# Kernel optimization log

Hardware: AMD Instinct MI355X
Metric: run time of the kernel (lower is better)

The kernel has to match this reference:

```python
import jax, jax.numpy as jnp
import numpy as np

N = 100000   # nodes
E = 800000   # directed edges
IN = 256     # in_channels (== hidden, required by repo's vn MLP dims)
HID = 256    # hidden_channels
OUT = 40     # out_channels (arxiv classes)
EPS = 1e-5


def setup_inputs() -> dict:
    key = jax.random.key(0)
    ks = jax.random.split(key, 8)
    def nrm(k, shape, scale=0.05):
        return jax.random.normal(k, shape, dtype=jnp.float32) * scale
    return {
        "x": nrm(ks[0], (N, IN), 1.0),
        "edge_index": jax.random.randint(ks[1], (2, E), 0, N, dtype=jnp.int32),
        # GCNConv weights (PyG: x @ W, then normalized aggregation, then + bias)
        "W0": nrm(ks[2], (IN, HID)),  "b0": jnp.zeros((HID,), jnp.float32),
        "W1": nrm(ks[3], (HID, HID)), "b1": jnp.zeros((HID,), jnp.float32),
        "W2": nrm(ks[4], (HID, OUT)), "b2": jnp.zeros((OUT,), jnp.float32),
        # BatchNorm1d affine params (batch-stat math, training mode)
        "bn_g0": jnp.ones((HID,), jnp.float32), "bn_b0": jnp.zeros((HID,), jnp.float32),
        "bn_g1": jnp.ones((HID,), jnp.float32), "bn_b1": jnp.zeros((HID,), jnp.float32),
        # virtual node embedding (init to 0 per reset_parameters)
        "vn_emb": jnp.zeros((1, IN), jnp.float32),
        # mlp_vns[0]: Linear(IN,HID) + LayerNorm(HID) + ReLU
        "vn_W0": nrm(ks[5], (IN, HID)),  "vn_b0": jnp.zeros((HID,), jnp.float32),
        "ln_g0": jnp.ones((HID,), jnp.float32), "ln_b0": jnp.zeros((HID,), jnp.float32),
        # mlp_vns[1]: Linear(HID,HID) + LayerNorm(HID) + ReLU
        "vn_W1": nrm(ks[6], (HID, HID)), "vn_b1": jnp.zeros((HID,), jnp.float32),
        "ln_g1": jnp.ones((HID,), jnp.float32), "ln_b1": jnp.zeros((HID,), jnp.float32),
    }


def _forward(x, edge_index, W0, b0, W1, b1, W2, b2, bn_g0, bn_b0, bn_g1, bn_b1,
             vn_emb, vn_W0, vn_b0, ln_g0, ln_b0, vn_W1, vn_b1, ln_g1, ln_b1):
    src, dst = edge_index[0], edge_index[1]
    # GCN symmetric normalization with self-loops: deg = in-degree + 1
    deg = jax.ops.segment_sum(jnp.ones(src.shape, jnp.float32), dst, num_segments=N) + 1.0
    dis = jax.lax.rsqrt(deg)                       # deg^{-1/2}  [N]
    coef = (dis[src] * dis[dst])[:, None]          # edge norm   [E,1]
    self_coef = (dis * dis)[:, None]               # self-loop norm = deg^{-1}  [N,1]

    def gcn(h, W, b):
        h = h @ W                                             # [N, out]
        agg = jax.ops.segment_sum(h[src] * coef, dst, num_segments=N)
        return agg + h * self_coef + b

    def bn(h, g, bv):  # BatchNorm1d, batch statistics over nodes
        mu = h.mean(0)
        var = ((h - mu) ** 2).mean(0)
        return (h - mu) * jax.lax.rsqrt(var + EPS) * g + bv

    def ln(h, g, bv):  # LayerNorm over last dim
        mu = h.mean(-1, keepdims=True)
        var = ((h - mu) ** 2).mean(-1, keepdims=True)
        return (h - mu) * jax.lax.rsqrt(var + EPS) * g + bv

    vx = vn_emb                                   # [1, IN]
    # layer 0
    h = x + vx                                    # virtual-node broadcast
    h = gcn(h, W0, b0)
    h = jax.nn.relu(bn(h, bn_g0, bn_b0))          # dropout = identity (eval)
    pool = jnp.sum(h, axis=0, keepdims=True)      # global_add_pool
    vx = jax.nn.relu(ln((pool + vx) @ vn_W0 + vn_b0, ln_g0, ln_b0))
    # layer 1
    h = h + vx
    h = gcn(h, W1, b1)
    h = jax.nn.relu(bn(h, bn_g1, bn_b1))
    pool = jnp.sum(h, axis=0, keepdims=True)
    vx = jax.nn.relu(ln((pool + vx) @ vn_W1 + vn_b1, ln_g1, ln_b1))
    # layer 2 (output)
    h = h + vx
    h = gcn(h, W2, b2)
    return jax.nn.log_softmax(h, axis=-1)


def reference(x, edge_index, W0, b0, W1, b1, W2, b2, bn_g0, bn_b0, bn_g1, bn_b1,
              vn_emb, vn_W0, vn_b0, ln_g0, ln_b0, vn_W1, vn_b1, ln_g1, ln_b1):
    return _forward(x, edge_index, W0, b0, W1, b1, W2, b2, bn_g0, bn_b0, bn_g1, bn_b1,
                    vn_emb, vn_W0, vn_b0, ln_g0, ln_b0, vn_W1, vn_b1, ln_g1, ln_b1)
```

## Files before the change

kernel.cpp:

```cpp
#include <hip/hip_runtime.h>
#include <hip/hip_bf16.h>
#include <cstdint>

#define N_NODES 100000
#define N_EDGES 800000
#define CH      256
#define COUT    40
#define COUTP   48
#define EPS     1e-5f
#define SCAN_CHUNK 1024
#define NSCAN_BLK  98
#define SB_NBLK 500
#define SB_ROWS 200
#define AGG_NPW 16

typedef unsigned short u16;
typedef unsigned int   u32;
typedef short s16x8 __attribute__((ext_vector_type(8)));
typedef float f32x4 __attribute__((ext_vector_type(4)));

__device__ __forceinline__ float b2f(u32 u) { return __uint_as_float(u << 16); }
__device__ __forceinline__ u16 f2b(float f) {
    u32 u = __float_as_uint(f);
    u32 r = (u + 0x7fffu + ((u >> 16) & 1u)) >> 16;
    return (u16)r;
}
__device__ __forceinline__ u32 packb(float a, float b) {
    return (u32)f2b(a) | ((u32)f2b(b) << 16);
}
__device__ __forceinline__ void unpack8(uint4 v, float* f) {
    f[0] = b2f(v.x & 0xffffu); f[1] = b2f(v.x >> 16);
    f[2] = b2f(v.y & 0xffffu); f[3] = b2f(v.y >> 16);
    f[4] = b2f(v.z & 0xffffu); f[5] = b2f(v.z >> 16);
    f[6] = b2f(v.w & 0xffffu); f[7] = b2f(v.w >> 16);
}

__global__ void k_count(const int* __restrict__ dst, int* __restrict__ counts) {
    int e = blockIdx.x * 256 + threadIdx.x;
    if (e < N_EDGES) atomicAdd(&counts[dst[e]], 1);
}

__global__ void k_scan1(const int* __restrict__ counts, int* __restrict__ partial,
                        int* __restrict__ blocksums) {
    __shared__ int sdata[256];
    int base = blockIdx.x * SCAN_CHUNK;
    int t = threadIdx.x;
    int v[4]; int s = 0;
    for (int j = 0; j < 4; j++) {
        int i = base + t * 4 + j;
        v[j] = (i < N_NODES) ? counts[i] : 0;
        s += v[j];
    }
    sdata[t] = s; __syncthreads();
    for (int off = 1; off < 256; off <<= 1) {
        int x = (t >= off) ? sdata[t - off] : 0;
        __syncthreads();
        sdata[t] += x;
        __syncthreads();
    }
    int incl = sdata[t];
    int run = incl - s;
    if (t == 255) blocksums[blockIdx.x] = incl;
    for (int j = 0; j < 4; j++) {
        int i = base + t * 4 + j;
        if (i < N_NODES) partial[i] = run;
        run += v[j];
    }
}

__global__ void k_scan2(int* __restrict__ blocksums) {
    __shared__ int sd[128];
    int t = threadIdx.x;
    int v = (t < NSCAN_BLK) ? blocksums[t] : 0;
    sd[t] = v; __syncthreads();
    for (int off = 1; off < 128; off <<= 1) {
        int x = (t >= off) ? sd[t - off] : 0;
        __syncthreads();
        sd[t] += x;
        __syncthreads();
    }
    if (t < NSCAN_BLK) blocksums[t] = sd[t] - v;
}

__global__ void k_scan3(int* __restrict__ row_start, const int* __restrict__ blocksums,
                        int* __restrict__ cursor) {
    int i = blockIdx.x * 256 + threadIdx.x;
    if (i < N_NODES) {
        int v = row_start[i] + blocksums[i >> 10];
        row_start[i] = v;
        cursor[i] = v;
    }
}

__global__ void k_dis(const int* __restrict__ counts, float* __restrict__ dis) {
    int i = blockIdx.x * 256 + threadIdx.x;
    if (i < N_NODES) dis[i] = rsqrtf(1.0f + (float)counts[i]);
}

__global__ void k_fill(const int* __restrict__ src, const int* __restrict__ dst,
                       int* __restrict__ cursor, int* __restrict__ csr,
                       const float* __restrict__ dis, float* __restrict__ coefv) {
    int e = blockIdx.x * 256 + threadIdx.x;
    if (e < N_EDGES) {
        int d = dst[e], s = src[e];
        int p = atomicAdd(&cursor[d], 1);
        csr[p] = s;
        coefv[p] = dis[s] * dis[d];
    }
}

__global__ void k_wt(const float* __restrict__ W, u16* __restrict__ Wt, int ncols) {
    int n = blockIdx.x, k = threadIdx.x;
    float v = (n < ncols) ? W[k * ncols + n] : 0.f;
    Wt[n * 256 + k] = f2b(v);
}

__global__ void k_xconv(const float* __restrict__ x, u16* __restrict__ xb) {
    int idx = (blockIdx.x * 256 + threadIdx.x) * 8;
    float4 a = *(const float4*)(x + idx);
    float4 b = *(const float4*)(x + idx + 4);
    uint4 o = {packb(a.x, a.y), packb(a.z, a.w), packb(b.x, b.y), packb(b.z, b.w)};
    *(uint4*)(xb + idx) = o;
}

__global__ void k_vecmat(const float* __restrict__ vec, const float* __restrict__ W,
                         int ncols, int npad, float* __restrict__ outv) {
    __shared__ float s[256];
    int t = threadIdx.x;
    s[t] = vec[t];
    __syncthreads();
    float acc = 0.f;
    if (t < ncols) {
        for (int k = 0; k < 256; k++) acc += s[k] * W[k * ncols + t];
    }
    if (t < npad) outv[t] = acc;
}

__global__ __launch_bounds__(256) void k_gemm(const u16* __restrict__ A,
                                              const u16* __restrict__ Wt,
                                              u16* __restrict__ Hout) {
    __shared__ u16 Bs[256 * 40];
    const int t = threadIdx.x;
    const int wave = t >> 6, lane = t & 63;
    const int lm = lane & 15, quad = lane >> 4;
    const int m0 = blockIdx.x * 64;
    const f32x4 vz = {0.f, 0.f, 0.f, 0.f};
    f32x4 acc[4][4];
    for (int m = 0; m < 4; m++)
        for (int c = 0; c < 4; c++) acc[m][c] = vz;

    for (int k0 = 0; k0 < 256; k0 += 32) {
        {
            const uint4* srcp = (const uint4*)(Wt + t * 256 + k0);
            uint4* dl = (uint4*)(Bs + t * 40);
            dl[0] = srcp[0]; dl[1] = srcp[1]; dl[2] = srcp[2]; dl[3] = srcp[3];
        }
        __syncthreads();
        s16x8 afrag[4];
#pragma unroll
        for (int m = 0; m < 4; m++) {
            int row = m0 + m * 16 + lm;
            if (row < N_NODES) afrag[m] = *(const s16x8*)(A + (size_t)row * 256 + k0 + quad * 8);
            else { s16x8 z = {0,0,0,0,0,0,0,0}; afrag[m] = z; }
        }
#pragma unroll
        for (int c = 0; c < 4; c++) {
            s16x8 bfrag = *(const s16x8*)(Bs + (wave * 64 + c * 16 + lm) * 40 + quad * 8);
#pragma unroll
            for (int m = 0; m < 4; m++)
                acc[m][c] = __builtin_amdgcn_mfma_f32_16x16x32_bf16(afrag[m], bfrag, acc[m][c], 0, 0, 0);
        }
        __syncthreads();
    }
#pragma unroll
    for (int m = 0; m < 4; m++) {
#pragma unroll
        for (int c = 0; c < 4; c++) {
            int col = wave * 64 + c * 16 + lm;
#pragma unroll
            for (int i = 0; i < 4; i++) {
                int row = m0 + m * 16 + quad * 4 + i;
                if (row < N_NODES) Hout[(size_t)row * 256 + col] = f2b(acc[m][c][i]);
            }
        }
    }
}

__global__ __launch_bounds__(256) void k_gemm2(const u16* __restrict__ A,
                                               const u16* __restrict__ Wt,
                                               u16* __restrict__ Hout) {
    __shared__ u16 Bs[48 * 40];
    const int t = threadIdx.x;
    const int wave = t >> 6, lane = t & 63;
    const int lm = lane & 15, quad = lane >> 4;
    const int m0 = blockIdx.x * 64;
    const f32x4 vz = {0.f, 0.f, 0.f, 0.f};
    f32x4 acc[3]; acc[0] = vz; acc[1] = vz; acc[2] = vz;

    for (int k0 = 0; k0 < 256; k0 += 32) {
        if (t < 48) {
            const uint4* srcp = (const uint4*)(Wt + t * 256 + k0);
            uint4* dl = (uint4*)(Bs + t * 40);
            dl[0] = srcp[0]; dl[1] = srcp[1]; dl[2] = srcp[2]; dl[3] = srcp[3];
        }
        __syncthreads();
        int row = m0 + wave * 16 + lm;
        s16x8 af;
        if (row < N_NODES) af = *(const s16x8*)(A + (size_t)row * 256 + k0 + quad * 8);
        else { s16x8 z = {0,0,0,0,0,0,0,0}; af = z; }
#pragma unroll
        for (int c = 0; c < 3; c++) {
            s16x8 bf = *(const s16x8*)(Bs + (c * 16 + lm) * 40 + quad * 8);
            acc[c] = __builtin_amdgcn_mfma_f32_16x16x32_bf16(af, bf, acc[c], 0, 0, 0);
        }
        __syncthreads();
    }
#pragma unroll
    for (int c = 0; c < 3; c++) {
        int col = c * 16 + lm;
#pragma unroll
        for (int i = 0; i < 4; i++) {
            int row = m0 + wave * 16 + quad * 4 + i;
            if (row < N_NODES) Hout[(size_t)row * COUTP + col] = f2b(acc[c][i]);
        }
    }
}

__global__ __launch_bounds__(256) void k_agg(const u16* __restrict__ H2,
                                             const int* __restrict__ row_start,
                                             const int* __restrict__ counts,
                                             const int* __restrict__ csr,
                                             const float* __restrict__ coefv,
                                             const float* __restrict__ dis,
                                             const float* __restrict__ bias,
                                             const float* __restrict__ v2,
                                             u16* __restrict__ OutB,
                                             float* __restrict__ stats) {
    __shared__ float ls[512];
    const int t = threadIdx.x, wave = t >> 6, lane = t & 63, ci = lane * 4;
    const float4 bb = *(const float4*)(bias + ci);
    const float4 vv = *(const float4*)(v2 + ci);
    float s0=0,s1=0,s2=0,s3=0,q0=0,q1=0,q2=0,q3=0;
    const int nbase = blockIdx.x * (4 * AGG_NPW) + wave * AGG_NPW;
    for (int i = 0; i < AGG_NPW; i++) {
        const int node = nbase + i;
        if (node >= N_NODES) break;
        const int beg = row_start[node], cnt = counts[node];
        const float dn = dis[node];
        float a0=0,a1=0,a2=0,a3=0, cs=0;
        int e = 0;
        for (; e + 4 <= cnt; e += 4) {
            int ia = csr[beg+e], ib = csr[beg+e+1], ic = csr[beg+e+2], id = csr[beg+e+3];
            float ca = coefv[beg+e], cb = coefv[beg+e+1], cc = coefv[beg+e+2], cd = coefv[beg+e+3];
            uint2 ra = *(const uint2*)(H2 + (size_t)ia * 256 + ci);
            uint2 rb = *(const uint2*)(H2 + (size_t)ib * 256 + ci);
            uint2 rc = *(const uint2*)(H2 + (size_t)ic * 256 + ci);
            uint2 rd = *(const uint2*)(H2 + (size_t)id * 256 + ci);
            cs += ca + cb + cc + cd;
            a0 += ca*b2f(ra.x&0xffffu) + cb*b2f(rb.x&0xffffu) + cc*b2f(rc.x&0xffffu) + cd*b2f(rd.x&0xffffu);
            a1 += ca*b2f(ra.x>>16)     + cb*b2f(rb.x>>16)     + cc*b2f(rc.x>>16)     + cd*b2f(rd.x>>16);
            a2 += ca*b2f(ra.y&0xffffu) + cb*b2f(rb.y&0xffffu) + cc*b2f(rc.y&0xffffu) + cd*b2f(rd.y&0xffffu);
            a3 += ca*b2f(ra.y>>16)     + cb*b2f(rb.y>>16)     + cc*b2f(rc.y>>16)     + cd*b2f(rd.y>>16);
        }
        for (; e < cnt; e++) {
            int ia = csr[beg+e]; float ca = coefv[beg+e];
            uint2 ra = *(const uint2*)(H2 + (size_t)ia * 256 + ci);
            cs += ca;
            a0 += ca*b2f(ra.x&0xffffu); a1 += ca*b2f(ra.x>>16);
            a2 += ca*b2f(ra.y&0xffffu); a3 += ca*b2f(ra.y>>16);
        }
        uint2 rs = *(const uint2*)(H2 + (size_t)node * 256 + ci);
        const float sc = dn * dn, cv = cs + sc;
        float f0 = a0 + sc*b2f(rs.x&0xffffu) + cv*vv.x + bb.x;
        float f1 = a1 + sc*b2f(rs.x>>16)     + cv*vv.y + bb.y;
        float f2 = a2 + sc*b2f(rs.y&0xffffu) + cv*vv.z + bb.z;
        float f3 = a3 + sc*b2f(rs.y>>16)     + cv*vv.w + bb.w;
        uint2 o; o.x = packb(f0, f1); o.y = packb(f2, f3);
        *(uint2*)(OutB + (size_t)node * 256 + ci) = o;
        s0 += f0; q0 += f0*f0; s1 += f1; q1 += f1*f1;
        s2 += f2; q2 += f2*f2; s3 += f3; q3 += f3*f3;
    }
    ls[t] = 0.f; ls[256 + t] = 0.f;
    __syncthreads();
    atomicAdd(&ls[ci], s0);   atomicAdd(&ls[ci+1], s1);
    atomicAdd(&ls[ci+2], s2); atomicAdd(&ls[ci+3], s3);
    atomicAdd(&ls[256+ci], q0);   atomicAdd(&ls[256+ci+1], q1);
    atomicAdd(&ls[256+ci+2], q2); atomicAdd(&ls[256+ci+3], q3);
    __syncthreads();
    atomicAdd(&stats[t], ls[t]);
    atomicAdd(&stats[256 + t], ls[256 + t]);
}

__global__ void k_fin(const float* __restrict__ stats, const float* __restrict__ g,
                      const float* __restrict__ bb, float* __restrict__ ggbc) {
    int t = threadIdx.x;
    const float inv = 1.0f / (float)N_NODES;
    float mu = stats[t] * inv;
    float var = stats[256 + t] * inv - mu * mu;
    float rs = rsqrtf(var + EPS);
    float gg = g[t] * rs;
    ggbc[t] = gg;
    ggbc[256 + t] = bb[t] - mu * gg;
}

__global__ __launch_bounds__(256) void k_bnrelu(const u16* __restrict__ OutB,
                                                const float* __restrict__ ggbc,
                                                u16* __restrict__ Hr,
                                                float* __restrict__ pool) {
    __shared__ float lp[256];
    const int t = threadIdx.x;
    const int cg = (t & 31) * 8;
    const int rg = t >> 5;
    const int r0 = blockIdx.x * SB_ROWS + rg;
    float gg[8], bc[8];
    {
        float4 a = *(const float4*)(ggbc + cg);
        float4 b = *(const float4*)(ggbc + cg + 4);
        float4 c = *(const float4*)(ggbc + 256 + cg);
        float4 d = *(const float4*)(ggbc + 256 + cg + 4);
        gg[0]=a.x; gg[1]=a.y; gg[2]=a.z; gg[3]=a.w; gg[4]=b.x; gg[5]=b.y; gg[6]=b.z; gg[7]=b.w;
        bc[0]=c.x; bc[1]=c.y; bc[2]=c.z; bc[3]=c.w; bc[4]=d.x; bc[5]=d.y; bc[6]=d.z; bc[7]=d.w;
    }
    float ps[8];
#pragma unroll
    for (int j = 0; j < 8; j++) ps[j] = 0.f;
#pragma unroll 2
    for (int it = 0; it < SB_ROWS / 8; it++) {
        int r = r0 + it * 8;
        uint4 v = *(const uint4*)(OutB + (size_t)r * 256 + cg);
        float f[8]; unpack8(v, f);
#pragma unroll
        for (int j = 0; j < 8; j++) {
            f[j] = fmaxf(f[j] * gg[j] + bc[j], 0.f);
            ps[j] += f[j];
        }
        uint4 o = {packb(f[0], f[1]), packb(f[2], f[3]), packb(f[4], f[5]), packb(f[6], f[7])};
        *(uint4*)(Hr + (size_t)r * 256 + cg) = o;
    }
    lp[t] = 0.f;
    __syncthreads();
#pragma unroll
    for (int j = 0; j < 8; j++) atomicAdd(&lp[cg + j], ps[j]);
    __syncthreads();
    atomicAdd(&pool[t], lp[t]);
}

__global__ void k_vx(const float* __restrict__ pool, const float* __restrict__ vx_old,
                     const float* __restrict__ vnW, const float* __restrict__ vnb,
                     const float* __restrict__ lng, const float* __restrict__ lnb,
                     float* __restrict__ vx_new,
                     const float* __restrict__ Wnext, int ncn, int npn,
                     float* __restrict__ v2n) {
    __shared__ float s[256];
    __shared__ float red[256];
    int t = threadIdx.x;
    s[t] = pool[t] + vx_old[t];
    __syncthreads();
    float y = vnb[t];
    for (int k = 0; k < 256; k++) y += s[k] * vnW[k * 256 + t];
    red[t] = y; __syncthreads();
    for (int off = 128; off > 0; off >>= 1) {
        if (t < off) red[t] += red[t + off];
        __syncthreads();
    }
    float mu = red[0] * (1.f / 256.f);
    __syncthreads();
    float d = y - mu;
    red[t] = d * d; __syncthreads();
    for (int off = 128; off > 0; off >>= 1) {
        if (t < off) red[t] += red[t + off];
        __syncthreads();
    }
    float var = red[0] * (1.f / 256.f);
    float v = fmaxf(d * rsqrtf(var + EPS) * lng[t] + lnb[t], 0.f);
    vx_new[t] = v;
    __syncthreads();
    s[t] = v;
    __syncthreads();
    float acc = 0.f;
    if (t < ncn) {
        for (int k = 0; k < 256; k++) acc += s[k] * Wnext[k * ncn + t];
    }
    if (t < npn) v2n[t] = acc;
}

__global__ __launch_bounds__(256) void k_agg2(const u16* __restrict__ H2,
                                              const int* __restrict__ row_start,
                                              const int* __restrict__ counts,
                                              const int* __restrict__ csr,
                                              const float* __restrict__ coefv,
                                              const float* __restrict__ dis,
                                              const float* __restrict__ bias,
                                              const float* __restrict__ v2,
                                              float* __restrict__ OutF) {
    const int t = threadIdx.x, wave = t >> 6, lane = t & 63;
    const int half = lane >> 5, hl = lane & 31;
    const bool gact = hl < 24;
    const bool cact = hl < 20;
    const int c0 = 2 * hl;
    float bb0 = 0.f, bb1 = 0.f, vv0 = 0.f, vv1 = 0.f;
    if (cact) {
        float2 bv = *(const float2*)(bias + c0); bb0 = bv.x; bb1 = bv.y;
        float2 vvv = *(const float2*)(v2 + c0);  vv0 = vvv.x; vv1 = vvv.y;
    }
    const int nbase = blockIdx.x * 16 + wave * 4;
    for (int i = 0; i < 4; i++) {
        const int node = nbase + i;
        const int beg = row_start[node], cnt = counts[node];
        const float dn = dis[node];
        float a0 = 0.f, a1 = 0.f, cs = 0.f;
        int e = half;
        for (; e + 6 < cnt; e += 8) {
            int ia = csr[beg+e], ib = csr[beg+e+2], ic = csr[beg+e+4], id = csr[beg+e+6];
            float ca = coefv[beg+e], cb = coefv[beg+e+2], cc = coefv[beg+e+4], cd = coefv[beg+e+6];
            u32 ra = 0, rb = 0, rc = 0, rd = 0;
            if (gact) {
                ra = *(const u32*)(H2 + (size_t)ia * COUTP + c0);
                rb = *(const u32*)(H2 + (size_t)ib * COUTP + c0);
                rc = *(const u32*)(H2 + (size_t)ic * COUTP + c0);
                rd = *(const u32*)(H2 + (size_t)id * COUTP + c0);
            }
            cs += ca + cb + cc + cd;
            a0 += ca*b2f(ra&0xffffu) + cb*b2f(rb&0xffffu) + cc*b2f(rc&0xffffu) + cd*b2f(rd&0xffffu);
            a1 += ca*b2f(ra>>16)     + cb*b2f(rb>>16)     + cc*b2f(rc>>16)     + cd*b2f(rd>>16);
        }
        for (; e < cnt; e += 2) {
            int ia = csr[beg+e]; float ca = coefv[beg+e];
            u32 ra = gact ? *(const u32*)(H2 + (size_t)ia * COUTP + c0) : 0u;
            cs += ca;
            a0 += ca*b2f(ra&0xffffu); a1 += ca*b2f(ra>>16);
        }
        a0 += __shfl_xor(a0, 32);
        a1 += __shfl_xor(a1, 32);
        cs += __shfl_xor(cs, 32);
        const float sc = dn * dn;
        u32 rs_ = gact ? *(const u32*)(H2 + (size_t)node * COUTP + c0) : 0u;
        float h0 = a0 + sc*b2f(rs_&0xffffu) + (cs+sc)*vv0 + bb0;
        float h1 = a1 + sc*b2f(rs_>>16)     + (cs+sc)*vv1 + bb1;
        float m = cact ? fmaxf(h0, h1) : -3.0e38f;
#pragma unroll
        for (int off = 16; off > 0; off >>= 1) m = fmaxf(m, __shfl_xor(m, off));
        float ex = cact ? (expf(h0 - m) + expf(h1 - m)) : 0.f;
        float se = ex;
#pragma unroll
        for (int off = 16; off > 0; off >>= 1) se += __shfl_xor(se, off);
        float lg = logf(se);
        if (cact && half == 0) {
            float2 o = {h0 - m - lg, h1 - m - lg};
            *(float2*)(OutF + (size_t)node * COUT + c0) = o;
        }
    }
}

extern "C" void kernel_launch(void* const* d_in, const int* in_sizes, int n_in,
                              void* d_out, int out_size, void* d_ws, size_t ws_size,
                              hipStream_t stream) {
    const float* x   = (const float*)d_in[0];
    const int*   ei  = (const int*)d_in[1];
    const int*   esrc = ei;
    const int*   edst = ei + N_EDGES;
    const float* W0 = (const float*)d_in[2];  const float* b0 = (const float*)d_in[3];
    const float* W1 = (const float*)d_in[4];  const float* b1 = (const float*)d_in[5];
    const float* W2 = (const float*)d_in[6];  const float* b2 = (const float*)d_in[7];
    const float* bg0 = (const float*)d_in[8]; const float* bb0 = (const float*)d_in[9];
    const float* bg1 = (const float*)d_in[10]; const float* bb1 = (const float*)d_in[11];
    const float* vn_emb = (const float*)d_in[12];
    const float* vW0 = (const float*)d_in[13]; const float* vb0 = (const float*)d_in[14];
    const float* lg0 = (const float*)d_in[15]; const float* lb0 = (const float*)d_in[16];
    const float* vW1 = (const float*)d_in[17]; const float* vb1 = (const float*)d_in[18];
    const float* lg1 = (const float*)d_in[19]; const float* lb1 = (const float*)d_in[20];

    char* w = (char*)d_ws;
    auto alloc = [&](size_t bytes) { void* p = (void*)w; w += ((bytes + 255) / 256) * 256; return p; };
    u16* H2    = (u16*)alloc((size_t)N_NODES * 256 * 2);
    u16* HR    = (u16*)alloc((size_t)N_NODES * 256 * 2);
    u16* OutB  = (u16*)alloc((size_t)N_NODES * 256 * 2);
    int* csr   = (int*)alloc((size_t)N_EDGES * 4);
    float* coefv = (float*)alloc((size_t)N_EDGES * 4);
    int* counts = (int*)alloc((size_t)N_NODES * 4);
    int* rowst  = (int*)alloc((size_t)N_NODES * 4);
    int* cursor = (int*)alloc((size_t)N_NODES * 4);
    float* dis  = (float*)alloc((size_t)N_NODES * 4);
    u16* Wtb0 = (u16*)alloc(256 * 256 * 2);
    u16* Wtb1 = (u16*)alloc(256 * 256 * 2);
    u16* Wt2b = (u16*)alloc(COUTP * 256 * 2);
    int* scanblk = (int*)alloc(128 * 4);
    float* stats = (float*)alloc(768 * 4);
    float* ggbc  = (float*)alloc(512 * 4);
    float* vxA = (float*)alloc(256 * 4);
    float* vxB = (float*)alloc(256 * 4);
    float* v20 = (float*)alloc(256 * 4);
    float* v21 = (float*)alloc(256 * 4);
    float* v22 = (float*)alloc(64 * 4);
    (void)ws_size; (void)in_sizes; (void)n_in; (void)out_size; (void)vxB;

    hipMemsetAsync(counts, 0, (size_t)N_NODES * 4, stream);
    k_count<<<(N_EDGES + 255) / 256, 256, 0, stream>>>(edst, counts);
    k_dis<<<(N_NODES + 255) / 256, 256, 0, stream>>>(counts, dis);
    k_scan1<<<NSCAN_BLK, 256, 0, stream>>>(counts, rowst, scanblk);
    k_scan2<<<1, 128, 0, stream>>>(scanblk);
    k_scan3<<<(N_NODES + 255) / 256, 256, 0, stream>>>(rowst, scanblk, cursor);
    k_fill<<<(N_EDGES + 255) / 256, 256, 0, stream>>>(esrc, edst, cursor, csr, dis, coefv);

    k_wt<<<256, 256, 0, stream>>>(W0, Wtb0, 256);
    k_wt<<<256, 256, 0, stream>>>(W1, Wtb1, 256);
    k_wt<<<COUTP, 256, 0, stream>>>(W2, Wt2b, COUT);
    k_xconv<<<(N_NODES * 256 / 8 + 255) / 256, 256, 0, stream>>>(x, HR);
    k_vecmat<<<1, 256, 0, stream>>>(vn_emb, W0, 256, 256, v20);

    const int aggblk = (N_NODES + 63) / 64;

    k_gemm<<<(N_NODES + 63) / 64, 256, 0, stream>>>(HR, Wtb0, H2);
    hipMemsetAsync(stats, 0, 768 * 4, stream);
    k_agg<<<aggblk, 256, 0, stream>>>(H2, rowst, counts, csr, coefv, dis, b0, v20, OutB, stats);
    k_fin<<<1, 256, 0, stream>>>(stats, bg0, bb0, ggbc);
    k_bnrelu<<<SB_NBLK, 256, 0, stream>>>(OutB, ggbc, HR, stats + 512);
    k_vx<<<1, 256, 0, stream>>>(stats + 512, vn_emb, vW0, vb0, lg0, lb0, vxA, W1, 256, 256, v21);

    k_gemm<<<(N_NODES + 63) / 64, 256, 0, stream>>>(HR, Wtb1, H2);
    hipMemsetAsync(stats, 0, 768 * 4, stream);
    k_agg<<<aggblk, 256, 0, stream>>>(H2, rowst, counts, csr, coefv, dis, b1, v21, OutB, stats);
    k_fin<<<1, 256, 0, stream>>>(stats, bg1, bb1, ggbc);
    k_bnrelu<<<SB_NBLK, 256, 0, stream>>>(OutB, ggbc, HR, stats + 512);
    k_vx<<<1, 256, 0, stream>>>(stats + 512, vxA, vW1, vb1, lg1, lb1, vxB, W2, COUT, COUTP, v22);

    k_gemm2<<<(N_NODES + 63) / 64, 256, 0, stream>>>(HR, Wt2b, H2);
    k_agg2<<<N_NODES / 16, 256, 0, stream>>>(H2, rowst, counts, csr, coefv, dis, b2, v22, (float*)d_out);
}
```

Baseline: 833.0 us.

## Fuse small setup kernels and stage GEMM A tiles through shared memory

Several small launches are folded into neighbours. The degree-rsqrt step moves into the scan finalisation, the three weight transposes become one launch, and the BN finalise step is recomputed inside each bnrelu block. Separately, both GEMM kernels now use a K-step of 64 and load the A tile cooperatively into padded LDS instead of reading it straight from global memory per wave. This cuts launch overhead and the number of barriers, in exchange for more LDS per block and redundant BN stat math in every block.

```diff
diff --git a/kernel.cpp b/kernel.cpp
--- a/kernel.cpp
+++ b/kernel.cpp
@@ -83,18 +83,15 @@
 }
 
 __global__ void k_scan3(int* __restrict__ row_start, const int* __restrict__ blocksums,
-                        int* __restrict__ cursor) {
+                        int* __restrict__ cursor, const int* __restrict__ counts,
+                        float* __restrict__ dis) {
     int i = blockIdx.x * 256 + threadIdx.x;
     if (i < N_NODES) {
         int v = row_start[i] + blocksums[i >> 10];
         row_start[i] = v;
         cursor[i] = v;
-    }
-}
-
-__global__ void k_dis(const int* __restrict__ counts, float* __restrict__ dis) {
-    int i = blockIdx.x * 256 + threadIdx.x;
-    if (i < N_NODES) dis[i] = rsqrtf(1.0f + (float)counts[i]);
+        dis[i] = rsqrtf(1.0f + (float)counts[i]);
+    }
 }
 
 __global__ void k_fill(const int* __restrict__ src, const int* __restrict__ dst,
@@ -109,10 +106,19 @@
     }
 }
 
-__global__ void k_wt(const float* __restrict__ W, u16* __restrict__ Wt, int ncols) {
-    int n = blockIdx.x, k = threadIdx.x;
-    float v = (n < ncols) ? W[k * ncols + n] : 0.f;
-    Wt[n * 256 + k] = f2b(v);
+__global__ void k_wt3(const float* __restrict__ W0, const float* __restrict__ W1,
+                      const float* __restrict__ W2,
+                      u16* __restrict__ T0, u16* __restrict__ T1, u16* __restrict__ T2) {
+    int b = blockIdx.x, k = threadIdx.x;
+    if (b < 256) {
+        T0[b * 256 + k] = f2b(W0[k * 256 + b]);
+    } else if (b < 512) {
+        int n = b - 256;
+        T1[n * 256 + k] = f2b(W1[k * 256 + n]);
+    } else {
+        int n = b - 512;
+        T2[n * 256 + k] = f2b(n < COUT ? W2[k * COUT + n] : 0.f);
+    }
 }
 
 __global__ void k_xconv(const float* __restrict__ x, u16* __restrict__ xb) {
@@ -139,36 +145,48 @@
 __global__ __launch_bounds__(256) void k_gemm(const u16* __restrict__ A,
                                               const u16* __restrict__ Wt,
                                               u16* __restrict__ Hout) {
-    __shared__ u16 Bs[256 * 40];
+    __shared__ u16 Bs[256 * 72];
+    __shared__ u16 As[64 * 72];
     const int t = threadIdx.x;
     const int wave = t >> 6, lane = t & 63;
     const int lm = lane & 15, quad = lane >> 4;
     const int m0 = blockIdx.x * 64;
+    const int ar = t >> 2, as_ = (t & 3) * 16;
+    const int arow = m0 + ar;
     const f32x4 vz = {0.f, 0.f, 0.f, 0.f};
     f32x4 acc[4][4];
     for (int m = 0; m < 4; m++)
         for (int c = 0; c < 4; c++) acc[m][c] = vz;
 
-    for (int k0 = 0; k0 < 256; k0 += 32) {
+    for (int k0 = 0; k0 < 256; k0 += 64) {
         {
-            const uint4* srcp = (const uint4*)(Wt + t * 256 + k0);
-            uint4* dl = (uint4*)(Bs + t * 40);
-            dl[0] = srcp[0]; dl[1] = srcp[1]; dl[2] = srcp[2]; dl[3] = srcp[3];
-        }
-        __syncthreads();
-        s16x8 afrag[4];
-#pragma unroll
-        for (int m = 0; m < 4; m++) {
-            int row = m0 + m * 16 + lm;
-            if (row < N_NODES) afrag[m] = *(const s16x8*)(A + (size_t)row * 256 + k0 + quad * 8);
-            else { s16x8 z = {0,0,0,0,0,0,0,0}; afrag[m] = z; }
-        }
-#pragma unroll
-        for (int c = 0; c < 4; c++) {
-            s16x8 bfrag = *(const s16x8*)(Bs + (wave * 64 + c * 16 + lm) * 40 + quad * 8);
+            const uint4* bsrc = (const uint4*)(Wt + t * 256 + k0);
+            uint4* bdst = (uint4*)(Bs + t * 72);
+#pragma unroll
+            for (int j = 0; j < 8; j++) bdst[j] = bsrc[j];
+            uint4 a0v = {0,0,0,0}, a1v = {0,0,0,0};
+            if (arow < N_NODES) {
+                const uint4* asrc = (const uint4*)(A + (size_t)arow * 256 + k0 + as_);
+                a0v = asrc[0]; a1v = asrc[1];
+            }
+            uint4* adst = (uint4*)(As + ar * 72 + as_);
+            adst[0] = a0v; adst[1] = a1v;
+        }
+        __syncthreads();
+#pragma unroll
+        for (int kk = 0; kk < 64; kk += 32) {
+            s16x8 af[4], bf[4];
 #pragma unroll
             for (int m = 0; m < 4; m++)
-                acc[m][c] = __builtin_amdgcn_mfma_f32_16x16x32_bf16(afrag[m], bfrag, acc[m][c], 0, 0, 0);
+                af[m] = *(const s16x8*)(As + (m * 16 + lm) * 72 + kk + quad * 8);
+#pragma unroll
+            for (int c = 0; c < 4; c++)
+                bf[c] = *(const s16x8*)(Bs + (wave * 64 + c * 16 + lm) * 72 + kk + quad * 8);
+#pragma unroll
+            for (int c = 0; c < 4; c++)
+#pragma unroll
+                for (int m = 0; m < 4; m++)
+                    acc[m][c] = __builtin_amdgcn_mfma_f32_16x16x32_bf16(af[m], bf[c], acc[m][c], 0, 0, 0);
         }
         __syncthreads();
     }
@@ -189,29 +207,42 @@
 __global__ __launch_bounds__(256) void k_gemm2(const u16* __restrict__ A,
                                                const u16* __restrict__ Wt,
                                                u16* __restrict__ Hout) {
-    __shared__ u16 Bs[48 * 40];
+    __shared__ u16 Bs[48 * 72];
+    __shared__ u16 As[64 * 72];
     const int t = threadIdx.x;
     const int wave = t >> 6, lane = t & 63;
     const int lm = lane & 15, quad = lane >> 4;
     const int m0 = blockIdx.x * 64;
+    const int ar = t >> 2, as_ = (t & 3) * 16;
+    const int arow = m0 + ar;
     const f32x4 vz = {0.f, 0.f, 0.f, 0.f};
     f32x4 acc[3]; acc[0] = vz; acc[1] = vz; acc[2] = vz;
 
-    for (int k0 = 0; k0 < 256; k0 += 32) {
-        if (t < 48) {
-            const uint4* srcp = (const uint4*)(Wt + t * 256 + k0);
-            uint4* dl = (uint4*)(Bs + t * 40);
-            dl[0] = srcp[0]; dl[1] = srcp[1]; dl[2] = srcp[2]; dl[3] = srcp[3];
-        }
-        __syncthreads();
-        int row = m0 + wave * 16 + lm;
-        s16x8 af;
-        if (row < N_NODES) af = *(const s16x8*)(A + (size_t)row * 256 + k0 + quad * 8);
-        else { s16x8 z = {0,0,0,0,0,0,0,0}; af = z; }
-#pragma unroll
-        for (int c = 0; c < 3; c++) {
-            s16x8 bf = *(const s16x8*)(Bs + (c * 16 + lm) * 40 + quad * 8);
-            acc[c] = __builtin_amdgcn_mfma_f32_16x16x32_bf16(af, bf, acc[c], 0, 0, 0);
+    for (int k0 = 0; k0 < 256; k0 += 64) {
+        {
+            if (t < 48) {
+                const uint4* bsrc = (const uint4*)(Wt + t * 256 + k0);
+                uint4* bdst = (uint4*)(Bs + t * 72);
+#pragma unroll
+                for (int j = 0; j < 8; j++) bdst[j] = bsrc[j];
+            }
+            uint4 a0v = {0,0,0,0}, a1v = {0,0,0,0};
+            if (arow < N_NODES) {
+                const uint4* asrc = (const uint4*)(A + (size_t)arow * 256 + k0 + as_);
+                a0v = asrc[0]; a1v = asrc[1];
+            }
+            uint4* adst = (uint4*)(As + ar * 72 + as_);
+            adst[0] = a0v; adst[1] = a1v;
+        }
+        __syncthreads();
+#pragma unroll
+        for (int kk = 0; kk < 64; kk += 32) {
+            s16x8 af = *(const s16x8*)(As + (wave * 16 + lm) * 72 + kk + quad * 8);
+#pragma unroll
+            for (int c = 0; c < 3; c++) {
+                s16x8 bf = *(const s16x8*)(Bs + (c * 16 + lm) * 72 + kk + quad * 8);
+                acc[c] = __builtin_amdgcn_mfma_f32_16x16x32_bf16(af, bf, acc[c], 0, 0, 0);
+            }
         }
         __syncthreads();
     }
@@ -291,20 +322,10 @@
     atomicAdd(&stats[256 + t], ls[256 + t]);
 }
 
-__global__ void k_fin(const float* __restrict__ stats, const float* __restrict__ g,
-                      const float* __restrict__ bb, float* __restrict__ ggbc) {
-    int t = threadIdx.x;
-    const float inv = 1.0f / (float)N_NODES;
-    float mu = stats[t] * inv;
-    float var = stats[256 + t] * inv - mu * mu;
-    float rs = rsqrtf(var + EPS);
-    float gg = g[t] * rs;
-    ggbc[t] = gg;
-    ggbc[256 + t] = bb[t] - mu * gg;
-}
-
 __global__ __launch_bounds__(256) void k_bnrelu(const u16* __restrict__ OutB,
-                                                const float* __restrict__ ggbc,
+                                                const float* __restrict__ stats,
+                                                const float* __restrict__ g,
+                                                const float* __restrict__ bb_,
                                                 u16* __restrict__ Hr,
                                                 float* __restrict__ pool) {
     __shared__ float lp[256];
@@ -312,14 +333,16 @@
     const int cg = (t & 31) * 8;
     const int rg = t >> 5;
     const int r0 = blockIdx.x * SB_ROWS + rg;
+    const float inv = 1.0f / (float)N_NODES;
     float gg[8], bc[8];
-    {
-        float4 a = *(const float4*)(ggbc + cg);
-        float4 b = *(const float4*)(ggbc + cg + 4);
-        float4 c = *(const float4*)(ggbc + 256 + cg);
-        float4 d = *(const float4*)(ggbc + 256 + cg + 4);
-        gg[0]=a.x; gg[1]=a.y; gg[2]=a.z; gg[3]=a.w; gg[4]=b.x; gg[5]=b.y; gg[6]=b.z; gg[7]=b.w;
-        bc[0]=c.x; bc[1]=c.y; bc[2]=c.z; bc[3]=c.w; bc[4]=d.x; bc[5]=d.y; bc[6]=d.z; bc[7]=d.w;
+#pragma unroll
+    for (int j = 0; j < 8; j++) {
+        int c = cg + j;
+        float mu = stats[c] * inv;
+        float var = stats[256 + c] * inv - mu * mu;
+        float rs = rsqrtf(var + EPS);
+        gg[j] = g[c] * rs;
+        bc[j] = bb_[c] - mu * gg[j];
     }
     float ps[8];
 #pragma unroll
@@ -486,7 +509,6 @@
     u16* Wt2b = (u16*)alloc(COUTP * 256 * 2);
     int* scanblk = (int*)alloc(128 * 4);
     float* stats = (float*)alloc(768 * 4);
-    float* ggbc  = (float*)alloc(512 * 4);
     float* vxA = (float*)alloc(256 * 4);
     float* vxB = (float*)alloc(256 * 4);
     float* v20 = (float*)alloc(256 * 4);
@@ -496,15 +518,12 @@
 
     hipMemsetAsync(counts, 0, (size_t)N_NODES * 4, stream);
     k_count<<<(N_EDGES + 255) / 256, 256, 0, stream>>>(edst, counts);
-    k_dis<<<(N_NODES + 255) / 256, 256, 0, stream>>>(counts, dis);
     k_scan1<<<NSCAN_BLK, 256, 0, stream>>>(counts, rowst, scanblk);
     k_scan2<<<1, 128, 0, stream>>>(scanblk);
-    k_scan3<<<(N_NODES + 255) / 256, 256, 0, stream>>>(rowst, scanblk, cursor);
+    k_scan3<<<(N_NODES + 255) / 256, 256, 0, stream>>>(rowst, scanblk, cursor, counts, dis);
     k_fill<<<(N_EDGES + 255) / 256, 256, 0, stream>>>(esrc, edst, cursor, csr, dis, coefv);
 
-    k_wt<<<256, 256, 0, stream>>>(W0, Wtb0, 256);
-    k_wt<<<256, 256, 0, stream>>>(W1, Wtb1, 256);
-    k_wt<<<COUTP, 256, 0, stream>>>(W2, Wt2b, COUT);
+    k_wt3<<<512 + COUTP, 256, 0, stream>>>(W0, W1, W2, Wtb0, Wtb1, Wt2b);
     k_xconv<<<(N_NODES * 256 / 8 + 255) / 256, 256, 0, stream>>>(x, HR);
     k_vecmat<<<1, 256, 0, stream>>>(vn_emb, W0, 256, 256, v20);
 
@@ -513,15 +532,13 @@
     k_gemm<<<(N_NODES + 63) / 64, 256, 0, stream>>>(HR, Wtb0, H2);
     hipMemsetAsync(stats, 0, 768 * 4, stream);
     k_agg<<<aggblk, 256, 0, stream>>>(H2, rowst, counts, csr, coefv, dis, b0, v20, OutB, stats);
-    k_fin<<<1, 256, 0, stream>>>(stats, bg0, bb0, ggbc);
-    k_bnrelu<<<SB_NBLK, 256, 0, stream>>>(OutB, ggbc, HR, stats + 512);
+    k_bnrelu<<<SB_NBLK, 256, 0, stream>>>(OutB, stats, bg0, bb0, HR, stats + 512);
     k_vx<<<1, 256, 0, stream>>>(stats + 512, vn_emb, vW0, vb0, lg0, lb0, vxA, W1, 256, 256, v21);
 
     k_gemm<<<(N_NODES + 63) / 64, 256, 0, stream>>>(HR, Wtb1, H2);
     hipMemsetAsync(stats, 0, 768 * 4, stream);
     k_agg<<<aggblk, 256, 0, stream>>>(H2, rowst, counts, csr, coefv, dis, b1, v21, OutB, stats);
-    k_fin<<<1, 256, 0, stream>>>(stats, bg1, bb1, ggbc);
-    k_bnrelu<<<SB_NBLK, 256, 0, stream>>>(OutB, ggbc, HR, stats + 512);
+    k_bnrelu<<<SB_NBLK, 256, 0, stream>>>(OutB, stats, bg1, bb1, HR, stats + 512);
     k_vx<<<1, 256, 0, stream>>>(stats + 512, vxA, vW1, vb1, lg1, lb1, vxB, W2, COUT, COUTP, v22);
 
     k_gemm2<<<(N_NODES + 63) / 64, 256, 0, stream>>>(HR, Wt2b, H2);
```

Measured after the change: 785.9 us. -5.7%, faster.
